# Kernel tuning notes

Hardware: AMD Instinct MI355X
Metric: run time of the kernel (lower is better)

## Reference

```python
import jax, jax.numpy as jnp
import numpy as np

D = 128      # dim_hidden
L = 8        # topological levels (level 0 = primary inputs)
M = 32768    # nodes per level
N = L * M
G = 5        # gate types: maj/not/and/or/xor -> 5 param sets
F = 2        # fan-in per gate node


def setup_inputs() -> dict:
    key = jax.random.key(0)
    ks = jax.random.split(key, 18)
    p = lambda k, sh: jax.random.normal(k, sh, jnp.float32) * 0.05
    return {
        's': jax.random.normal(ks[0], (N, D), jnp.float32),
        't': jax.random.normal(ks[1], (N, D), jnp.float32),
        'gate': jax.random.randint(ks[2], (N,), 0, G, jnp.int32),
        'fanin': jax.random.randint(ks[3], (L - 1, M, F), 0, M, jnp.int32),
        'hs_W': p(ks[4], (2 * D, D)), 'hs_b': p(ks[5], (D,)),
        'aggr_W1': p(ks[6], (G, 2 * D, D)), 'aggr_b1': p(ks[7], (G, D)),
        'aggr_W2': p(ks[8], (G, D, D)), 'aggr_b2': p(ks[9], (G, D)),
        'aggr_W3': p(ks[10], (G, D, D)), 'aggr_b3': p(ks[11], (G, D)),
        'gru_Wi': p(ks[12], (G, D, 3 * D)), 'gru_Wh': p(ks[13], (G, D, 3 * D)),
        'gru_bi': p(ks[14], (G, 3 * D)), 'gru_bh': p(ks[15], (G, 3 * D)),
    }


def _forward(s, t, gate, fanin, hs_W, hs_b, aggr_W1, aggr_b1, aggr_W2, aggr_b2,
             aggr_W3, aggr_b3, gru_Wi, gru_Wh, gru_bi, gru_bh):
    hs = jnp.concatenate([s, t], -1) @ hs_W + hs_b          # [N,D]
    hf = jnp.zeros((N, D), hs.dtype)                        # functional state, zero-init
    for lvl in range(1, L):                                 # level-synchronous sweep
        lo = lvl * M
        g_l = gate[lo:lo + M]                               # [M] gate type of dst nodes
        oh = jax.nn.one_hot(g_l, G, dtype=hs.dtype)         # [M,G] gate selector
        src = (lvl - 1) * M + fanin[lvl - 1]                # [M,F] global fan-in indices
        src_state = jnp.concatenate([hs[src], hf[src]], -1)  # [M,F,2D] node_state gather
        # per-gate-type edge MLP (TFMlpAggr): 3-layer MLP on source states, sum over fan-in
        h1 = jax.nn.relu(jnp.einsum('mfc,gcd->gmfd', src_state, aggr_W1) + aggr_b1[:, None, None, :])
        h2 = jax.nn.relu(jnp.einsum('gmfd,gde->gmfe', h1, aggr_W2) + aggr_b2[:, None, None, :])
        m = jnp.einsum('gmfe,gek->gmfk', h2, aggr_W3) + aggr_b3[:, None, None, :]
        msg = jnp.einsum('gmd,mg->md', m.sum(axis=2), oh)   # [M,D] select own gate's aggr
        # per-gate-type GRU update of hf (torch GRU math, seq_len=1)
        h = hf[lo:lo + M]                                   # [M,D]
        gi = jnp.einsum('md,gdk->gmk', msg, gru_Wi) + gru_bi[:, None, :]  # [G,M,3D]
        gh = jnp.einsum('md,gdk->gmk', h, gru_Wh) + gru_bh[:, None, :]
        r = jax.nn.sigmoid(gi[..., :D] + gh[..., :D])
        z = jax.nn.sigmoid(gi[..., D:2 * D] + gh[..., D:2 * D])
        n = jnp.tanh(gi[..., 2 * D:] + r * gh[..., 2 * D:])
        h_new = jnp.einsum('gmd,mg->md', (1.0 - z) * n + z * h[None], oh)
        hf = hf.at[lo:lo + M].set(h_new)                    # scatter-write back
    return hs, hf


def reference(s, t, gate, fanin, hs_W, hs_b, aggr_W1, aggr_b1, aggr_W2, aggr_b2,
              aggr_W3, aggr_b3, gru_Wi, gru_Wh, gru_bi, gru_bh):
    return _forward(s, t, gate, fanin, hs_W, hs_b, aggr_W1, aggr_b1, aggr_W2,
                    aggr_b2, aggr_W3, aggr_b3, gru_Wi, gru_Wh, gru_bi, gru_bh)
```

## Files before the change

kernel.cpp:

```cpp
#include <hip/hip_runtime.h>
#include <hip/hip_bf16.h>

#define DD 128
#define LL 8
#define MM 32768
#define NN (LL*MM)
#define GG 5
#define FF 2
#define SORT_STRIDE 33408

typedef __attribute__((ext_vector_type(8))) short short8;
typedef __attribute__((ext_vector_type(4))) short short4v;
typedef __attribute__((ext_vector_type(4))) float f32x4;

#define MFMA16(a,b,c) __builtin_amdgcn_mfma_f32_16x16x32_bf16((a),(b),(c),0,0,0)

__device__ __forceinline__ short f2bf(float x){
  __hip_bfloat16 h = __float2bfloat16(x);
  return *reinterpret_cast<short*>(&h);
}

__device__ __forceinline__ short8 pack8(f32x4 a, f32x4 b){
  short8 r;
  r[0]=f2bf(a[0]); r[1]=f2bf(a[1]); r[2]=f2bf(a[2]); r[3]=f2bf(a[3]);
  r[4]=f2bf(b[0]); r[5]=f2bf(b[1]); r[6]=f2bf(b[2]); r[7]=f2bf(b[3]);
  return r;
}

__global__ void prep_kernel(const float* __restrict__ hs_W, const float* __restrict__ W1,
                            const float* __restrict__ W2, const float* __restrict__ W3,
                            const float* __restrict__ Wi,
                            short* __restrict__ hsWt, short* __restrict__ W1t,
                            short* __restrict__ W2t, short* __restrict__ W3t,
                            short* __restrict__ Wit, int* __restrict__ cntcur)
{
  if (blockIdx.x == 0 && threadIdx.x < 70) cntcur[threadIdx.x] = 0;
  int u = blockIdx.x*256 + threadIdx.x;
  const float* src; short* dst; int ldw;
  if (u < 4096){
    int i=u, ct=i>>9, kc=(i>>6)&7, lane=i&63;
    src = hs_W + (size_t)(kc*32 + 8*(lane>>4))*128 + ct*16 + (lane&15);
    dst = hsWt + (size_t)i*8; ldw=128;
  } else if (u < 24576){
    int v=u-4096, g=v>>12, i=v&4095, ct=i>>9, kc=(i>>6)&7, lane=i&63;
    src = W1 + (size_t)g*32768 + (size_t)(kc*32 + 8*(lane>>4))*128 + ct*16 + (lane&15);
    dst = W1t + (size_t)g*32768 + i*8; ldw=128;
  } else if (u < 34816){
    int v=u-24576, g=v>>11, i=v&2047, ct=i>>8, kc=(i>>6)&3, lane=i&63;
    src = W2 + (size_t)g*16384 + (size_t)(kc*32 + 8*(lane>>4))*128 + ct*16 + (lane&15);
    dst = W2t + (size_t)g*16384 + i*8; ldw=128;
  } else if (u < 45056){
    int v=u-34816, g=v>>11, i=v&2047, ct=i>>8, kc=(i>>6)&3, lane=i&63;
    src = W3 + (size_t)g*16384 + (size_t)(kc*32 + 8*(lane>>4))*128 + ct*16 + (lane&15);
    dst = W3t + (size_t)g*16384 + i*8; ldw=128;
  } else {
    int v=u-45056, g=v/6144, i=v%6144, ct=i>>8, kc=(i>>6)&3, lane=i&63;
    src = Wi + (size_t)g*49152 + (size_t)(kc*32 + 8*(lane>>4))*384 + ct*16 + (lane&15);
    dst = Wit + (size_t)g*49152 + i*8; ldw=384;
  }
  short8 o;
#pragma unroll
  for (int j=0;j<8;++j) o[j] = f2bf(src[(size_t)j*ldw]);
  *(short8*)dst = o;
}

__global__ void count_kernel(const int* __restrict__ gate, int* __restrict__ cnt){
  __shared__ int lc[GG];
  const int li = blockIdx.x >> 7;
  const int m  = ((blockIdx.x & 127) << 8) + threadIdx.x;
  if (threadIdx.x < GG) lc[threadIdx.x] = 0;
  __syncthreads();
  int g = gate[(li+1)*MM + m];
  atomicAdd(&lc[g], 1);
  __syncthreads();
  if (threadIdx.x < GG && lc[threadIdx.x] > 0)
    atomicAdd(&cnt[li*GG + threadIdx.x], lc[threadIdx.x]);
}

__global__ void offs_kernel(const int* __restrict__ cnt, int* __restrict__ off,
                            int* __restrict__ pend, int* __restrict__ sorted){
  __shared__ int se[35], sp[35];
  const int tid = threadIdx.x;
  if (tid < LL-1){
    int l = tid, o = 0;
    for (int g = 0; g < GG; ++g){
      off[l*GG+g] = o;
      int c = cnt[l*GG+g];
      pend[l*GG+g] = o + c;
      se[l*GG+g] = o + c;
      o += ((c + 31) >> 5) << 5;
      sp[l*GG+g] = o;
    }
  }
  __syncthreads();
  for (int b = 0; b < 35; ++b){
    int l = b / GG;
    for (int i = se[b] + tid; i < sp[b]; i += 256)
      sorted[l*SORT_STRIDE + i] = -1;
  }
}

__global__ void scatter_kernel(const int* __restrict__ gate, const int* __restrict__ off,
                               int* __restrict__ cur, int* __restrict__ sorted){
  __shared__ int lc[GG];
  __shared__ int base[GG];
  const int li = blockIdx.x >> 7;
  const int m  = ((blockIdx.x & 127) << 8) + threadIdx.x;
  if (threadIdx.x < GG) lc[threadIdx.x] = 0;
  __syncthreads();
  int g = gate[(li+1)*MM + m];
  int p = atomicAdd(&lc[g], 1);
  __syncthreads();
  if (threadIdx.x < GG)
    base[threadIdx.x] = atomicAdd(&cur[li*GG + threadIdx.x], lc[threadIdx.x]);
  __syncthreads();
  sorted[li*SORT_STRIDE + off[li*GG+g] + base[g] + p] = m;
}

__global__ __launch_bounds__(256,4) void hs_kernel(
    const float* __restrict__ s, const float* __restrict__ t,
    const short* __restrict__ Wt, const float* __restrict__ b,
    float* __restrict__ hs, short* __restrict__ hs_sh,
    float* __restrict__ hf, short* __restrict__ hf_sh)
{
  __shared__ __align__(16) short Xs[16384];
  const int tid=threadIdx.x, lane=tid&63, w=tid>>6;
  const int l15=lane&15, lq=lane>>4;
  const int row0 = blockIdx.x*64;

  {
    const int r = tid>>2, p = tid&3;
    const float* srow = s + (size_t)(row0+r)*DD;
    const float* trow = t + (size_t)(row0+r)*DD;
    const int rf = r>>4, rl = r&15;
#pragma unroll
    for (int i=0;i<8;++i){
      int u = p + 4*i;
      const float* pp = (u<16) ? (srow + 8*u) : (trow + 8*(u-16));
      short8 v = pack8(*(const f32x4*)pp, *(const f32x4*)(pp+4));
      *(short8*)(Xs + ((rf*8+(u>>2))*64 + (u&3)*16 + rl)*8) = v;
    }
  }

  if (row0 < MM){
    f32x4 zf4 = {0.f,0.f,0.f,0.f};
    short8 zs8 = {0,0,0,0,0,0,0,0};
    const size_t basei = (size_t)row0*DD;
#pragma unroll
    for (int i=tid; i<2048; i+=256) *(f32x4*)(hf + basei + i*4) = zf4;
#pragma unroll
    for (int i=tid; i<1024; i+=256) *(short8*)(hf_sh + basei + i*8) = zs8;
  }
  __syncthreads();

  f32x4 zf = {0.f,0.f,0.f,0.f};
  f32x4 acc[4][2];
#pragma unroll
  for (int rr=0;rr<4;++rr){ acc[rr][0]=zf; acc[rr][1]=zf; }

  const short* Ab = Wt + lane*8;
#pragma unroll
  for (int kc=0;kc<8;++kc){
    short8 a0 = *(const short8*)(Ab + (16*w + kc)*512);
    short8 a1 = *(const short8*)(Ab + (16*w + 8 + kc)*512);
#pragma unroll
    for (int rr=0;rr<4;++rr){
      short8 bx = *(const short8*)(Xs + ((rr*8 + kc)*64 + lane)*8);
      acc[rr][0] = MFMA16(a0, bx, acc[rr][0]);
      acc[rr][1] = MFMA16(a1, bx, acc[rr][1]);
    }
  }

  f32x4 bv0 = *(const f32x4*)(b + 32*w + 4*lq);
  f32x4 bv1 = *(const f32x4*)(b + 32*w + 16 + 4*lq);
#pragma unroll
  for (int rr=0;rr<4;++rr){
    int row = row0 + rr*16 + l15;
#pragma unroll
    for (int q=0;q<2;++q){
      f32x4 bv = q ? bv1 : bv0;
      int col = 32*w + 16*q + 4*lq;
      f32x4 o; short4v pk;
#pragma unroll
      for (int j=0;j<4;++j){ o[j] = acc[rr][q][j] + bv[j]; pk[j] = f2bf(o[j]); }
      *(f32x4*)(hs + (size_t)row*DD + col) = o;
      *(short4v*)(hs_sh + (size_t)row*DD + col) = pk;
    }
  }
}

__global__ __launch_bounds__(256,4) void level_kernel(
    int lvl, float* __restrict__ hfg,
    const short* __restrict__ hs_sh, short* __restrict__ hf_sh,
    const int* __restrict__ fanin,
    const short* __restrict__ W1t, const short* __restrict__ W2t,
    const short* __restrict__ W3t, const short* __restrict__ Wit,
    const float* __restrict__ b1, const float* __restrict__ b2,
    const float* __restrict__ b3, const float* __restrict__ bi,
    const float* __restrict__ bh,
    const int* __restrict__ off, const int* __restrict__ pend,
    const int* __restrict__ sorted)
{
  __shared__ __align__(16) short Xs[16384];
  __shared__ int nodebuf[32];
  __shared__ int srcbuf[64];
  __shared__ int ginfo;

  const int tid=threadIdx.x, lane=tid&63, w=tid>>6;
  const int l15=lane&15, lq=lane>>4;
  const int li = lvl-1;
  const int pos0 = blockIdx.x*32;

  if (tid==0){
    int g=-1;
    for (int q=0;q<GG;++q)
      if (pos0>=off[li*GG+q] && pos0<pend[li*GG+q]){ g=q; break; }
    ginfo=g;
  }
  if (tid<32) nodebuf[tid] = sorted[li*SORT_STRIDE + pos0 + tid];
  if (tid<64){
    int mg = sorted[li*SORT_STRIDE + pos0 + (tid>>1)];
    srcbuf[tid] = (mg>=0) ? li*MM + fanin[((size_t)li*MM+mg)*FF + (tid&1)] : 0;
  }
  __syncthreads();
  const int g = ginfo;
  if (g<0) return;

  {
    const int r = tid>>2, p = tid&3;
    const int src = srcbuf[r];
    const short* hsrow = hs_sh + (size_t)src*DD;
    const short* hfrow = hf_sh + (size_t)src*DD;
    const int rf = r>>4, rl = r&15;
#pragma unroll
    for (int i=0;i<8;++i){
      int u = p + 4*i;
      short8 v = *(const short8*)((u<16) ? (hsrow + 8*u) : (hfrow + 8*(u-16)));
      *(short8*)(Xs + ((rf*8+(u>>2))*64 + (u&3)*16 + rl)*8) = v;
    }
  }
  __syncthreads();

  f32x4 zf = {0.f,0.f,0.f,0.f};

  f32x4 acc[4][2];
#pragma unroll
  for (int rr=0;rr<4;++rr){ acc[rr][0]=zf; acc[rr][1]=zf; }
  const short* A1 = W1t + (size_t)g*32768 + lane*8;
#pragma unroll
  for (int kc=0;kc<8;++kc){
    short8 a0 = *(const short8*)(A1 + (16*w + kc)*512);
    short8 a1 = *(const short8*)(A1 + (16*w + 8 + kc)*512);
#pragma unroll
    for (int rr=0;rr<4;++rr){
      short8 bx = *(const short8*)(Xs + ((rr*8 + kc)*64 + lane)*8);
      acc[rr][0] = MFMA16(a0, bx, acc[rr][0]);
      acc[rr][1] = MFMA16(a1, bx, acc[rr][1]);
    }
  }
  __syncthreads();
  {
    f32x4 bv0 = *(const f32x4*)(b1 + g*DD + 32*w + 4*lq);
    f32x4 bv1 = *(const f32x4*)(b1 + g*DD + 32*w + 16 + 4*lq);
#pragma unroll
    for (int rr=0;rr<4;++rr){
#pragma unroll
      for (int q=0;q<2;++q){
        f32x4 bv = q ? bv1 : bv0;
        short4v pk;
#pragma unroll
        for (int j=0;j<4;++j) pk[j] = f2bf(fmaxf(acc[rr][q][j] + bv[j], 0.f));
        *(short4v*)(Xs + ((rr*4 + w)*64 + (2*q + (lq>>1))*16 + l15)*8 + 4*(lq&1)) = pk;
      }
    }
  }
  __syncthreads();

  f32x4 acc2[4][2];
#pragma unroll
  for (int rr=0;rr<4;++rr){ acc2[rr][0]=zf; acc2[rr][1]=zf; }
  const short* A2 = W2t + (size_t)g*16384 + lane*8;
#pragma unroll
  for (int kc=0;kc<4;++kc){
    short8 a0 = *(const short8*)(A2 + (8*w + kc)*512);
    short8 a1 = *(const short8*)(A2 + (8*w + 4 + kc)*512);
#pragma unroll
    for (int rr=0;rr<4;++rr){
      short8 bx = *(const short8*)(Xs + ((rr*4 + kc)*64 + lane)*8);
      acc2[rr][0] = MFMA16(a0, bx, acc2[rr][0]);
      acc2[rr][1] = MFMA16(a1, bx, acc2[rr][1]);
    }
  }
  {
    f32x4 bv0 = *(const f32x4*)(b2 + g*DD + 32*w + 4*lq);
    f32x4 bv1 = *(const f32x4*)(b2 + g*DD + 32*w + 16 + 4*lq);
#pragma unroll
    for (int rr=0;rr<4;++rr){
#pragma unroll
      for (int q=0;q<2;++q){
        f32x4 bv = q ? bv1 : bv0;
        short4v pk;
#pragma unroll
        for (int j=0;j<4;++j) pk[j] = f2bf(fmaxf(acc2[rr][q][j] + bv[j], 0.f));
        *(short4v*)(Xs + 8192 + ((rr*4 + w)*64 + (2*q + (lq>>1))*16 + l15)*8 + 4*(lq&1)) = pk;
      }
    }
  }
  __syncthreads();

  f32x4 acc3[4][2];
#pragma unroll
  for (int rr=0;rr<4;++rr){ acc3[rr][0]=zf; acc3[rr][1]=zf; }
  const short* A3 = W3t + (size_t)g*16384 + lane*8;
#pragma unroll
  for (int kc=0;kc<4;++kc){
    short8 a0 = *(const short8*)(A3 + (8*w + kc)*512);
    short8 a1 = *(const short8*)(A3 + (8*w + 4 + kc)*512);
#pragma unroll
    for (int rr=0;rr<4;++rr){
      short8 bx = *(const short8*)(Xs + 8192 + ((rr*4 + kc)*64 + lane)*8);
      acc3[rr][0] = MFMA16(a0, bx, acc3[rr][0]);
      acc3[rr][1] = MFMA16(a1, bx, acc3[rr][1]);
    }
  }
  {
    f32x4 bv0 = *(const f32x4*)(b3 + g*DD + 32*w + 4*lq);
    f32x4 bv1 = *(const f32x4*)(b3 + g*DD + 32*w + 16 + 4*lq);
#pragma unroll
    for (int rr=0;rr<4;++rr){
#pragma unroll
      for (int q=0;q<2;++q){
        f32x4 bv = q ? bv1 : bv0;
        f32x4 mv;
#pragma unroll
        for (int j=0;j<4;++j){
          float v = acc3[rr][q][j];
          mv[j] = v + __shfl_xor(v, 1) + 2.f*bv[j];
        }
        if ((l15 & 1) == 0){
          int n = rr*8 + (l15>>1);
          short4v pk;
#pragma unroll
          for (int j=0;j<4;++j) pk[j] = f2bf(mv[j]);
          *(short4v*)(Xs + (((n>>4)*4 + w)*64 + (2*q + (lq>>1))*16 + (n&15))*8 + 4*(lq&1)) = pk;
        }
      }
    }
  }
  __syncthreads();

  const short* AW = Wit + (size_t)g*49152 + lane*8;
  const int lo = lvl*MM;
#pragma unroll
  for (int q=0;q<2;++q){
    f32x4 gr[2], gz[2], gn[2];
    gr[0]=zf; gr[1]=zf; gz[0]=zf; gz[1]=zf; gn[0]=zf; gn[1]=zf;
#pragma unroll
    for (int kc=0;kc<4;++kc){
      int cti = ((2*w + q)*4 + kc)*512;
      short8 aR = *(const short8*)(AW + cti);
      short8 aZ = *(const short8*)(AW + 16384 + cti);
      short8 aN = *(const short8*)(AW + 32768 + cti);
#pragma unroll
      for (int rfm=0;rfm<2;++rfm){
        short8 bm = *(const short8*)(Xs + ((rfm*4 + kc)*64 + lane)*8);
        gr[rfm] = MFMA16(aR, bm, gr[rfm]);
        gz[rfm] = MFMA16(aZ, bm, gz[rfm]);
        gn[rfm] = MFMA16(aN, bm, gn[rfm]);
      }
    }
    int col = 32*w + 16*q + 4*lq;
    f32x4 biR = *(const f32x4*)(bi + g*384 + col);
    f32x4 biZ = *(const f32x4*)(bi + g*384 + 128 + col);
    f32x4 biN = *(const f32x4*)(bi + g*384 + 256 + col);
    f32x4 bhR = *(const f32x4*)(bh + g*384 + col);
    f32x4 bhZ = *(const f32x4*)(bh + g*384 + 128 + col);
    f32x4 bhN = *(const f32x4*)(bh + g*384 + 256 + col);
#pragma unroll
    for (int rfm=0;rfm<2;++rfm){
      int m = nodebuf[rfm*16 + l15];
      if (m < 0) continue;
      f32x4 o; short4v pk;
#pragma unroll
      for (int j=0;j<4;++j){
        float xr = gr[rfm][j] + biR[j] + bhR[j];
        float xz = gz[rfm][j] + biZ[j] + bhZ[j];
        float r_ = 1.f/(1.f + __expf(-xr));
        float z_ = 1.f/(1.f + __expf(-xz));
        float xn = gn[rfm][j] + biN[j] + r_*bhN[j];
        float n_ = 2.f/(1.f + __expf(-2.f*xn)) - 1.f;
        o[j] = (1.f - z_)*n_;
        pk[j] = f2bf(o[j]);
      }
      *(f32x4*)(hfg + (size_t)(lo + m)*DD + col) = o;
      *(short4v*)(hf_sh + (size_t)(lo + m)*DD + col) = pk;
    }
  }
}

extern "C" void kernel_launch(void* const* d_in, const int* in_sizes, int n_in,
                              void* d_out, int out_size, void* d_ws, size_t ws_size,
                              hipStream_t stream)
{
  const float* s    = (const float*)d_in[0];
  const float* t    = (const float*)d_in[1];
  const int*   gate = (const int*)d_in[2];
  const int*   fanin= (const int*)d_in[3];
  const float* hs_W = (const float*)d_in[4];
  const float* hs_b = (const float*)d_in[5];
  const float* W1   = (const float*)d_in[6];
  const float* b1   = (const float*)d_in[7];
  const float* W2   = (const float*)d_in[8];
  const float* b2   = (const float*)d_in[9];
  const float* W3   = (const float*)d_in[10];
  const float* b3   = (const float*)d_in[11];
  const float* Wi   = (const float*)d_in[12];
  const float* bi   = (const float*)d_in[14];
  const float* bh   = (const float*)d_in[15];

  float* hs = (float*)d_out;
  float* hf = hs + (size_t)NN*DD;

  int* cnt    = (int*)d_ws;
  int* cur    = cnt + 35;
  int* off    = cnt + 70;
  int* pendv  = cnt + 105;
  int* sorted = cnt + 256;

  short* wbase = (short*)((char*)d_ws + (1<<20));
  short* hsWt = wbase;
  short* W1t  = wbase + 32768;
  short* W2t  = wbase + 196608;
  short* W3t  = wbase + 278528;
  short* Wit  = wbase + 360448;

  short* hs_sh = (short*)((char*)d_ws + (size_t)(8<<20));
  short* hf_sh = hs_sh + (size_t)NN*DD;

  prep_kernel<<<296, 256, 0, stream>>>(hs_W, W1, W2, W3, Wi,
                                       hsWt, W1t, W2t, W3t, Wit, cnt);
  count_kernel<<<896, 256, 0, stream>>>(gate, cnt);
  offs_kernel<<<1, 256, 0, stream>>>(cnt, off, pendv, sorted);
  scatter_kernel<<<896, 256, 0, stream>>>(gate, off, cur, sorted);
  hs_kernel<<<NN/64, 256, 0, stream>>>(s, t, hsWt, hs_b, hs, hs_sh, hf, hf_sh);
  for (int lvl = 1; lvl < LL; ++lvl){
    level_kernel<<<SORT_STRIDE/32, 256, 0, stream>>>(lvl, hf,
        hs_sh, hf_sh, fanin, W1t, W2t, W3t, Wit,
        b1, b2, b3, bi, bh, off, pendv, sorted);
  }
}
```

Before: 405.0 us.

## Fuse all stages into one persistent kernel with software grid barriers

Replaces the chain of prep, count, offsets, scatter, hs and seven per-level launches with a single persistent kernel. Blocks loop over work items and synchronise between dependent phases with an atomic-counter grid barrier. The goal is to remove per-launch overhead and inter-kernel gaps. The cost is spin-wait barriers, a fixed grid sized from occupancy, and a risk of deadlock if not all blocks are co-resident.

```diff
diff --git a/kernel.cpp b/kernel.cpp
--- a/kernel.cpp
+++ b/kernel.cpp
@@ -27,374 +27,371 @@
   return r;
 }
 
-__global__ void prep_kernel(const float* __restrict__ hs_W, const float* __restrict__ W1,
-                            const float* __restrict__ W2, const float* __restrict__ W3,
-                            const float* __restrict__ Wi,
-                            short* __restrict__ hsWt, short* __restrict__ W1t,
-                            short* __restrict__ W2t, short* __restrict__ W3t,
-                            short* __restrict__ Wit, int* __restrict__ cntcur)
-{
-  if (blockIdx.x == 0 && threadIdx.x < 70) cntcur[threadIdx.x] = 0;
-  int u = blockIdx.x*256 + threadIdx.x;
-  const float* src; short* dst; int ldw;
-  if (u < 4096){
-    int i=u, ct=i>>9, kc=(i>>6)&7, lane=i&63;
-    src = hs_W + (size_t)(kc*32 + 8*(lane>>4))*128 + ct*16 + (lane&15);
-    dst = hsWt + (size_t)i*8; ldw=128;
-  } else if (u < 24576){
-    int v=u-4096, g=v>>12, i=v&4095, ct=i>>9, kc=(i>>6)&7, lane=i&63;
-    src = W1 + (size_t)g*32768 + (size_t)(kc*32 + 8*(lane>>4))*128 + ct*16 + (lane&15);
-    dst = W1t + (size_t)g*32768 + i*8; ldw=128;
-  } else if (u < 34816){
-    int v=u-24576, g=v>>11, i=v&2047, ct=i>>8, kc=(i>>6)&3, lane=i&63;
-    src = W2 + (size_t)g*16384 + (size_t)(kc*32 + 8*(lane>>4))*128 + ct*16 + (lane&15);
-    dst = W2t + (size_t)g*16384 + i*8; ldw=128;
-  } else if (u < 45056){
-    int v=u-34816, g=v>>11, i=v&2047, ct=i>>8, kc=(i>>6)&3, lane=i&63;
-    src = W3 + (size_t)g*16384 + (size_t)(kc*32 + 8*(lane>>4))*128 + ct*16 + (lane&15);
-    dst = W3t + (size_t)g*16384 + i*8; ldw=128;
-  } else {
-    int v=u-45056, g=v/6144, i=v%6144, ct=i>>8, kc=(i>>6)&3, lane=i&63;
-    src = Wi + (size_t)g*49152 + (size_t)(kc*32 + 8*(lane>>4))*384 + ct*16 + (lane&15);
-    dst = Wit + (size_t)g*49152 + i*8; ldw=384;
-  }
-  short8 o;
-#pragma unroll
-  for (int j=0;j<8;++j) o[j] = f2bf(src[(size_t)j*ldw]);
-  *(short8*)dst = o;
+__device__ __forceinline__ void gbar(int* bar, int target){
+  __syncthreads();
+  if (threadIdx.x == 0){
+    __threadfence();
+    atomicAdd(bar, 1);
+    while (__hip_atomic_load(bar, __ATOMIC_ACQUIRE, __HIP_MEMORY_SCOPE_AGENT) < target)
+      __builtin_amdgcn_s_sleep(8);
+    __threadfence();
+  }
+  __syncthreads();
 }
 
-__global__ void count_kernel(const int* __restrict__ gate, int* __restrict__ cnt){
-  __shared__ int lc[GG];
-  const int li = blockIdx.x >> 7;
-  const int m  = ((blockIdx.x & 127) << 8) + threadIdx.x;
-  if (threadIdx.x < GG) lc[threadIdx.x] = 0;
-  __syncthreads();
-  int g = gate[(li+1)*MM + m];
-  atomicAdd(&lc[g], 1);
-  __syncthreads();
-  if (threadIdx.x < GG && lc[threadIdx.x] > 0)
-    atomicAdd(&cnt[li*GG + threadIdx.x], lc[threadIdx.x]);
-}
-
-__global__ void offs_kernel(const int* __restrict__ cnt, int* __restrict__ off,
-                            int* __restrict__ pend, int* __restrict__ sorted){
-  __shared__ int se[35], sp[35];
-  const int tid = threadIdx.x;
-  if (tid < LL-1){
-    int l = tid, o = 0;
-    for (int g = 0; g < GG; ++g){
-      off[l*GG+g] = o;
-      int c = cnt[l*GG+g];
-      pend[l*GG+g] = o + c;
-      se[l*GG+g] = o + c;
-      o += ((c + 31) >> 5) << 5;
-      sp[l*GG+g] = o;
-    }
-  }
-  __syncthreads();
-  for (int b = 0; b < 35; ++b){
-    int l = b / GG;
-    for (int i = se[b] + tid; i < sp[b]; i += 256)
-      sorted[l*SORT_STRIDE + i] = -1;
-  }
-}
-
-__global__ void scatter_kernel(const int* __restrict__ gate, const int* __restrict__ off,
-                               int* __restrict__ cur, int* __restrict__ sorted){
-  __shared__ int lc[GG];
-  __shared__ int base[GG];
-  const int li = blockIdx.x >> 7;
-  const int m  = ((blockIdx.x & 127) << 8) + threadIdx.x;
-  if (threadIdx.x < GG) lc[threadIdx.x] = 0;
-  __syncthreads();
-  int g = gate[(li+1)*MM + m];
-  int p = atomicAdd(&lc[g], 1);
-  __syncthreads();
-  if (threadIdx.x < GG)
-    base[threadIdx.x] = atomicAdd(&cur[li*GG + threadIdx.x], lc[threadIdx.x]);
-  __syncthreads();
-  sorted[li*SORT_STRIDE + off[li*GG+g] + base[g] + p] = m;
-}
-
-__global__ __launch_bounds__(256,4) void hs_kernel(
+__global__ __launch_bounds__(256,4) void mega_kernel(
     const float* __restrict__ s, const float* __restrict__ t,
-    const short* __restrict__ Wt, const float* __restrict__ b,
-    float* __restrict__ hs, short* __restrict__ hs_sh,
-    float* __restrict__ hf, short* __restrict__ hf_sh)
-{
-  __shared__ __align__(16) short Xs[16384];
-  const int tid=threadIdx.x, lane=tid&63, w=tid>>6;
-  const int l15=lane&15, lq=lane>>4;
-  const int row0 = blockIdx.x*64;
-
-  {
-    const int r = tid>>2, p = tid&3;
-    const float* srow = s + (size_t)(row0+r)*DD;
-    const float* trow = t + (size_t)(row0+r)*DD;
-    const int rf = r>>4, rl = r&15;
-#pragma unroll
-    for (int i=0;i<8;++i){
-      int u = p + 4*i;
-      const float* pp = (u<16) ? (srow + 8*u) : (trow + 8*(u-16));
-      short8 v = pack8(*(const f32x4*)pp, *(const f32x4*)(pp+4));
-      *(short8*)(Xs + ((rf*8+(u>>2))*64 + (u&3)*16 + rl)*8) = v;
-    }
-  }
-
-  if (row0 < MM){
-    f32x4 zf4 = {0.f,0.f,0.f,0.f};
-    short8 zs8 = {0,0,0,0,0,0,0,0};
-    const size_t basei = (size_t)row0*DD;
-#pragma unroll
-    for (int i=tid; i<2048; i+=256) *(f32x4*)(hf + basei + i*4) = zf4;
-#pragma unroll
-    for (int i=tid; i<1024; i+=256) *(short8*)(hf_sh + basei + i*8) = zs8;
-  }
-  __syncthreads();
-
-  f32x4 zf = {0.f,0.f,0.f,0.f};
-  f32x4 acc[4][2];
-#pragma unroll
-  for (int rr=0;rr<4;++rr){ acc[rr][0]=zf; acc[rr][1]=zf; }
-
-  const short* Ab = Wt + lane*8;
-#pragma unroll
-  for (int kc=0;kc<8;++kc){
-    short8 a0 = *(const short8*)(Ab + (16*w + kc)*512);
-    short8 a1 = *(const short8*)(Ab + (16*w + 8 + kc)*512);
-#pragma unroll
-    for (int rr=0;rr<4;++rr){
-      short8 bx = *(const short8*)(Xs + ((rr*8 + kc)*64 + lane)*8);
-      acc[rr][0] = MFMA16(a0, bx, acc[rr][0]);
-      acc[rr][1] = MFMA16(a1, bx, acc[rr][1]);
-    }
-  }
-
-  f32x4 bv0 = *(const f32x4*)(b + 32*w + 4*lq);
-  f32x4 bv1 = *(const f32x4*)(b + 32*w + 16 + 4*lq);
-#pragma unroll
-  for (int rr=0;rr<4;++rr){
-    int row = row0 + rr*16 + l15;
-#pragma unroll
-    for (int q=0;q<2;++q){
-      f32x4 bv = q ? bv1 : bv0;
-      int col = 32*w + 16*q + 4*lq;
-      f32x4 o; short4v pk;
-#pragma unroll
-      for (int j=0;j<4;++j){ o[j] = acc[rr][q][j] + bv[j]; pk[j] = f2bf(o[j]); }
-      *(f32x4*)(hs + (size_t)row*DD + col) = o;
-      *(short4v*)(hs_sh + (size_t)row*DD + col) = pk;
-    }
-  }
-}
-
-__global__ __launch_bounds__(256,4) void level_kernel(
-    int lvl, float* __restrict__ hfg,
-    const short* __restrict__ hs_sh, short* __restrict__ hf_sh,
-    const int* __restrict__ fanin,
-    const short* __restrict__ W1t, const short* __restrict__ W2t,
-    const short* __restrict__ W3t, const short* __restrict__ Wit,
-    const float* __restrict__ b1, const float* __restrict__ b2,
-    const float* __restrict__ b3, const float* __restrict__ bi,
+    const int* __restrict__ gate, const int* __restrict__ fanin,
+    const float* __restrict__ hs_W, const float* __restrict__ hs_b,
+    const float* __restrict__ W1, const float* __restrict__ b1,
+    const float* __restrict__ W2, const float* __restrict__ b2,
+    const float* __restrict__ W3, const float* __restrict__ b3,
+    const float* __restrict__ Wi, const float* __restrict__ bi,
     const float* __restrict__ bh,
-    const int* __restrict__ off, const int* __restrict__ pend,
-    const int* __restrict__ sorted)
+    float* __restrict__ hs, float* __restrict__ hf,
+    short* __restrict__ hsWt, short* __restrict__ W1t, short* __restrict__ W2t,
+    short* __restrict__ W3t, short* __restrict__ Wit,
+    short* __restrict__ hs_sh, short* __restrict__ hf_sh,
+    int* __restrict__ cnt, int* __restrict__ cur, int* __restrict__ off,
+    int* __restrict__ pend, int* __restrict__ pad_end,
+    int* __restrict__ sorted, int* __restrict__ bar)
 {
   __shared__ __align__(16) short Xs[16384];
   __shared__ int nodebuf[32];
   __shared__ int srcbuf[64];
   __shared__ int ginfo;
 
-  const int tid=threadIdx.x, lane=tid&63, w=tid>>6;
-  const int l15=lane&15, lq=lane>>4;
-  const int li = lvl-1;
-  const int pos0 = blockIdx.x*32;
-
-  if (tid==0){
-    int g=-1;
-    for (int q=0;q<GG;++q)
-      if (pos0>=off[li*GG+q] && pos0<pend[li*GG+q]){ g=q; break; }
-    ginfo=g;
-  }
-  if (tid<32) nodebuf[tid] = sorted[li*SORT_STRIDE + pos0 + tid];
-  if (tid<64){
-    int mg = sorted[li*SORT_STRIDE + pos0 + (tid>>1)];
-    srcbuf[tid] = (mg>=0) ? li*MM + fanin[((size_t)li*MM+mg)*FF + (tid&1)] : 0;
-  }
-  __syncthreads();
-  const int g = ginfo;
-  if (g<0) return;
-
-  {
-    const int r = tid>>2, p = tid&3;
-    const int src = srcbuf[r];
-    const short* hsrow = hs_sh + (size_t)src*DD;
-    const short* hfrow = hf_sh + (size_t)src*DD;
-    const int rf = r>>4, rl = r&15;
-#pragma unroll
-    for (int i=0;i<8;++i){
-      int u = p + 4*i;
-      short8 v = *(const short8*)((u<16) ? (hsrow + 8*u) : (hfrow + 8*(u-16)));
-      *(short8*)(Xs + ((rf*8+(u>>2))*64 + (u&3)*16 + rl)*8) = v;
-    }
-  }
-  __syncthreads();
-
+  const int blk = blockIdx.x, NB = gridDim.x;
+  const int tid = threadIdx.x, lane = tid & 63, w = tid >> 6;
+  const int l15 = lane & 15, lq = lane >> 4;
   f32x4 zf = {0.f,0.f,0.f,0.f};
 
-  f32x4 acc[4][2];
-#pragma unroll
-  for (int rr=0;rr<4;++rr){ acc[rr][0]=zf; acc[rr][1]=zf; }
-  const short* A1 = W1t + (size_t)g*32768 + lane*8;
-#pragma unroll
-  for (int kc=0;kc<8;++kc){
-    short8 a0 = *(const short8*)(A1 + (16*w + kc)*512);
-    short8 a1 = *(const short8*)(A1 + (16*w + 8 + kc)*512);
+  for (int u = blk*256 + tid; u < 75776; u += NB*256){
+    const float* src; short* dst; int ldw;
+    if (u < 4096){
+      int i=u, ct=i>>9, kc=(i>>6)&7, ln=i&63;
+      src = hs_W + (size_t)(kc*32 + 8*(ln>>4))*128 + ct*16 + (ln&15);
+      dst = hsWt + (size_t)i*8; ldw=128;
+    } else if (u < 24576){
+      int v=u-4096, g=v>>12, i=v&4095, ct=i>>9, kc=(i>>6)&7, ln=i&63;
+      src = W1 + (size_t)g*32768 + (size_t)(kc*32 + 8*(ln>>4))*128 + ct*16 + (ln&15);
+      dst = W1t + (size_t)g*32768 + i*8; ldw=128;
+    } else if (u < 34816){
+      int v=u-24576, g=v>>11, i=v&2047, ct=i>>8, kc=(i>>6)&3, ln=i&63;
+      src = W2 + (size_t)g*16384 + (size_t)(kc*32 + 8*(ln>>4))*128 + ct*16 + (ln&15);
+      dst = W2t + (size_t)g*16384 + i*8; ldw=128;
+    } else if (u < 45056){
+      int v=u-34816, g=v>>11, i=v&2047, ct=i>>8, kc=(i>>6)&3, ln=i&63;
+      src = W3 + (size_t)g*16384 + (size_t)(kc*32 + 8*(ln>>4))*128 + ct*16 + (ln&15);
+      dst = W3t + (size_t)g*16384 + i*8; ldw=128;
+    } else {
+      int v=u-45056, g=v/6144, i=v%6144, ct=i>>8, kc=(i>>6)&3, ln=i&63;
+      src = Wi + (size_t)g*49152 + (size_t)(kc*32 + 8*(ln>>4))*384 + ct*16 + (ln&15);
+      dst = Wit + (size_t)g*49152 + i*8; ldw=384;
+    }
+    short8 o;
+#pragma unroll
+    for (int j=0;j<8;++j) o[j] = f2bf(src[(size_t)j*ldw]);
+    *(short8*)dst = o;
+  }
+  for (int c0 = blk; c0 < 896; c0 += NB){
+    int* lc = (int*)Xs;
+    __syncthreads();
+    if (tid < GG) lc[tid] = 0;
+    __syncthreads();
+    int idx = c0*256 + tid;
+    int li = idx >> 15, m = idx & 32767;
+    int g = gate[(li+1)*MM + m];
+    atomicAdd(&lc[g], 1);
+    __syncthreads();
+    if (tid < GG && lc[tid] > 0) atomicAdd(&cnt[li*GG + tid], lc[tid]);
+  }
+  gbar(bar, NB*1);
+
+  if (blk < LL-1){
+    int* lds_i = (int*)Xs;
+    if (tid == 0){
+      int l = blk, o = 0;
+      for (int g2 = 0; g2 < GG; ++g2){
+        off[l*GG+g2] = o;
+        int c = cnt[l*GG+g2];
+        pend[l*GG+g2] = o + c;
+        lds_i[g2] = o + c;
+        o += ((c + 31) >> 5) << 5;
+        lds_i[8+g2] = o;
+      }
+      pad_end[l] = o;
+    }
+    __syncthreads();
+    for (int b2 = 0; b2 < GG; ++b2)
+      for (int i = lds_i[b2] + tid; i < lds_i[8+b2]; i += 256)
+        sorted[blk*SORT_STRIDE + i] = -1;
+  }
+  gbar(bar, NB*2);
+
+  for (int c0 = blk; c0 < 896; c0 += NB){
+    int* lc = (int*)Xs; int* base = lc + 8;
+    __syncthreads();
+    if (tid < GG) lc[tid] = 0;
+    __syncthreads();
+    int idx = c0*256 + tid;
+    int li = idx >> 15, m = idx & 32767;
+    int g = gate[(li+1)*MM + m];
+    int p = atomicAdd(&lc[g], 1);
+    __syncthreads();
+    if (tid < GG) base[tid] = atomicAdd(&cur[li*GG + tid], lc[tid]);
+    __syncthreads();
+    sorted[li*SORT_STRIDE + off[li*GG+g] + base[g] + p] = m;
+  }
+  for (int it = blk; it < 4096; it += NB){
+    const int row0 = it*64;
+    __syncthreads();
+    {
+      const int r = tid>>2, p = tid&3;
+      const float* srow = s + (size_t)(row0+r)*DD;
+      const float* trow = t + (size_t)(row0+r)*DD;
+      const int rf = r>>4, rl = r&15;
+#pragma unroll
+      for (int i=0;i<8;++i){
+        int u = p + 4*i;
+        const float* pp = (u<16) ? (srow + 8*u) : (trow + 8*(u-16));
+        short8 v = pack8(*(const f32x4*)pp, *(const f32x4*)(pp+4));
+        *(short8*)(Xs + ((rf*8+(u>>2))*64 + (u&3)*16 + rl)*8) = v;
+      }
+    }
+    if (row0 < MM){
+      short8 zs8 = {0,0,0,0,0,0,0,0};
+      const size_t basei = (size_t)row0*DD;
+      for (int i=tid; i<2048; i+=256) *(f32x4*)(hf + basei + i*4) = zf;
+      for (int i=tid; i<1024; i+=256) *(short8*)(hf_sh + basei + i*8) = zs8;
+    }
+    __syncthreads();
+
+    f32x4 acc[4][2];
+#pragma unroll
+    for (int rr=0;rr<4;++rr){ acc[rr][0]=zf; acc[rr][1]=zf; }
+    const short* Ab = hsWt + lane*8;
+#pragma unroll
+    for (int kc=0;kc<8;++kc){
+      short8 a0 = *(const short8*)(Ab + (16*w + kc)*512);
+      short8 a1 = *(const short8*)(Ab + (16*w + 8 + kc)*512);
+#pragma unroll
+      for (int rr=0;rr<4;++rr){
+        short8 bx = *(const short8*)(Xs + ((rr*8 + kc)*64 + lane)*8);
+        acc[rr][0] = MFMA16(a0, bx, acc[rr][0]);
+        acc[rr][1] = MFMA16(a1, bx, acc[rr][1]);
+      }
+    }
+    f32x4 bv0 = *(const f32x4*)(hs_b + 32*w + 4*lq);
+    f32x4 bv1 = *(const f32x4*)(hs_b + 32*w + 16 + 4*lq);
 #pragma unroll
     for (int rr=0;rr<4;++rr){
-      short8 bx = *(const short8*)(Xs + ((rr*8 + kc)*64 + lane)*8);
-      acc[rr][0] = MFMA16(a0, bx, acc[rr][0]);
-      acc[rr][1] = MFMA16(a1, bx, acc[rr][1]);
-    }
-  }
-  __syncthreads();
-  {
-    f32x4 bv0 = *(const f32x4*)(b1 + g*DD + 32*w + 4*lq);
-    f32x4 bv1 = *(const f32x4*)(b1 + g*DD + 32*w + 16 + 4*lq);
-#pragma unroll
-    for (int rr=0;rr<4;++rr){
+      int row = row0 + rr*16 + l15;
 #pragma unroll
       for (int q=0;q<2;++q){
         f32x4 bv = q ? bv1 : bv0;
-        short4v pk;
-#pragma unroll
-        for (int j=0;j<4;++j) pk[j] = f2bf(fmaxf(acc[rr][q][j] + bv[j], 0.f));
-        *(short4v*)(Xs + ((rr*4 + w)*64 + (2*q + (lq>>1))*16 + l15)*8 + 4*(lq&1)) = pk;
-      }
-    }
-  }
-  __syncthreads();
-
-  f32x4 acc2[4][2];
-#pragma unroll
-  for (int rr=0;rr<4;++rr){ acc2[rr][0]=zf; acc2[rr][1]=zf; }
-  const short* A2 = W2t + (size_t)g*16384 + lane*8;
-#pragma unroll
-  for (int kc=0;kc<4;++kc){
-    short8 a0 = *(const short8*)(A2 + (8*w + kc)*512);
-    short8 a1 = *(const short8*)(A2 + (8*w + 4 + kc)*512);
-#pragma unroll
-    for (int rr=0;rr<4;++rr){
-      short8 bx = *(const short8*)(Xs + ((rr*4 + kc)*64 + lane)*8);
-      acc2[rr][0] = MFMA16(a0, bx, acc2[rr][0]);
-      acc2[rr][1] = MFMA16(a1, bx, acc2[rr][1]);
-    }
-  }
-  {
-    f32x4 bv0 = *(const f32x4*)(b2 + g*DD + 32*w + 4*lq);
-    f32x4 bv1 = *(const f32x4*)(b2 + g*DD + 32*w + 16 + 4*lq);
-#pragma unroll
-    for (int rr=0;rr<4;++rr){
-#pragma unroll
-      for (int q=0;q<2;++q){
-        f32x4 bv = q ? bv1 : bv0;
-        short4v pk;
-#pragma unroll
-        for (int j=0;j<4;++j) pk[j] = f2bf(fmaxf(acc2[rr][q][j] + bv[j], 0.f));
-        *(short4v*)(Xs + 8192 + ((rr*4 + w)*64 + (2*q + (lq>>1))*16 + l15)*8 + 4*(lq&1)) = pk;
-      }
-    }
-  }
-  __syncthreads();
-
-  f32x4 acc3[4][2];
-#pragma unroll
-  for (int rr=0;rr<4;++rr){ acc3[rr][0]=zf; acc3[rr][1]=zf; }
-  const short* A3 = W3t + (size_t)g*16384 + lane*8;
-#pragma unroll
-  for (int kc=0;kc<4;++kc){
-    short8 a0 = *(const short8*)(A3 + (8*w + kc)*512);
-    short8 a1 = *(const short8*)(A3 + (8*w + 4 + kc)*512);
-#pragma unroll
-    for (int rr=0;rr<4;++rr){
-      short8 bx = *(const short8*)(Xs + 8192 + ((rr*4 + kc)*64 + lane)*8);
-      acc3[rr][0] = MFMA16(a0, bx, acc3[rr][0]);
-      acc3[rr][1] = MFMA16(a1, bx, acc3[rr][1]);
-    }
-  }
-  {
-    f32x4 bv0 = *(const f32x4*)(b3 + g*DD + 32*w + 4*lq);
-    f32x4 bv1 = *(const f32x4*)(b3 + g*DD + 32*w + 16 + 4*lq);
-#pragma unroll
-    for (int rr=0;rr<4;++rr){
-#pragma unroll
-      for (int q=0;q<2;++q){
-        f32x4 bv = q ? bv1 : bv0;
-        f32x4 mv;
-#pragma unroll
-        for (int j=0;j<4;++j){
-          float v = acc3[rr][q][j];
-          mv[j] = v + __shfl_xor(v, 1) + 2.f*bv[j];
-        }
-        if ((l15 & 1) == 0){
-          int n = rr*8 + (l15>>1);
-          short4v pk;
-#pragma unroll
-          for (int j=0;j<4;++j) pk[j] = f2bf(mv[j]);
-          *(short4v*)(Xs + (((n>>4)*4 + w)*64 + (2*q + (lq>>1))*16 + (n&15))*8 + 4*(lq&1)) = pk;
-        }
-      }
-    }
-  }
-  __syncthreads();
-
-  const short* AW = Wit + (size_t)g*49152 + lane*8;
-  const int lo = lvl*MM;
-#pragma unroll
-  for (int q=0;q<2;++q){
-    f32x4 gr[2], gz[2], gn[2];
-    gr[0]=zf; gr[1]=zf; gz[0]=zf; gz[1]=zf; gn[0]=zf; gn[1]=zf;
-#pragma unroll
-    for (int kc=0;kc<4;++kc){
-      int cti = ((2*w + q)*4 + kc)*512;
-      short8 aR = *(const short8*)(AW + cti);
-      short8 aZ = *(const short8*)(AW + 16384 + cti);
-      short8 aN = *(const short8*)(AW + 32768 + cti);
-#pragma unroll
-      for (int rfm=0;rfm<2;++rfm){
-        short8 bm = *(const short8*)(Xs + ((rfm*4 + kc)*64 + lane)*8);
-        gr[rfm] = MFMA16(aR, bm, gr[rfm]);
-        gz[rfm] = MFMA16(aZ, bm, gz[rfm]);
-        gn[rfm] = MFMA16(aN, bm, gn[rfm]);
-      }
-    }
-    int col = 32*w + 16*q + 4*lq;
-    f32x4 biR = *(const f32x4*)(bi + g*384 + col);
-    f32x4 biZ = *(const f32x4*)(bi + g*384 + 128 + col);
-    f32x4 biN = *(const f32x4*)(bi + g*384 + 256 + col);
-    f32x4 bhR = *(const f32x4*)(bh + g*384 + col);
-    f32x4 bhZ = *(const f32x4*)(bh + g*384 + 128 + col);
-    f32x4 bhN = *(const f32x4*)(bh + g*384 + 256 + col);
-#pragma unroll
-    for (int rfm=0;rfm<2;++rfm){
-      int m = nodebuf[rfm*16 + l15];
-      if (m < 0) continue;
-      f32x4 o; short4v pk;
-#pragma unroll
-      for (int j=0;j<4;++j){
-        float xr = gr[rfm][j] + biR[j] + bhR[j];
-        float xz = gz[rfm][j] + biZ[j] + bhZ[j];
-        float r_ = 1.f/(1.f + __expf(-xr));
-        float z_ = 1.f/(1.f + __expf(-xz));
-        float xn = gn[rfm][j] + biN[j] + r_*bhN[j];
-        float n_ = 2.f/(1.f + __expf(-2.f*xn)) - 1.f;
-        o[j] = (1.f - z_)*n_;
-        pk[j] = f2bf(o[j]);
-      }
-      *(f32x4*)(hfg + (size_t)(lo + m)*DD + col) = o;
-      *(short4v*)(hf_sh + (size_t)(lo + m)*DD + col) = pk;
-    }
+        int col = 32*w + 16*q + 4*lq;
+        f32x4 o; short4v pk;
+#pragma unroll
+        for (int j=0;j<4;++j){ o[j] = acc[rr][q][j] + bv[j]; pk[j] = f2bf(o[j]); }
+        *(f32x4*)(hs + (size_t)row*DD + col) = o;
+        *(short4v*)(hs_sh + (size_t)row*DD + col) = pk;
+      }
+    }
+  }
+  gbar(bar, NB*3);
+
+  for (int lvl = 1; lvl < LL; ++lvl){
+    const int li = lvl-1;
+    const int pe = pad_end[li];
+    for (int it = blk; it*32 < pe; it += NB){
+      const int pos0 = it*32;
+      __syncthreads();
+      if (tid==0){
+        int g=-1;
+        for (int q=0;q<GG;++q)
+          if (pos0>=off[li*GG+q] && pos0<pend[li*GG+q]){ g=q; break; }
+        ginfo=g;
+      }
+      if (tid<32) nodebuf[tid] = sorted[li*SORT_STRIDE + pos0 + tid];
+      if (tid<64){
+        int mg = sorted[li*SORT_STRIDE + pos0 + (tid>>1)];
+        srcbuf[tid] = (mg>=0) ? li*MM + fanin[((size_t)li*MM+mg)*FF + (tid&1)] : 0;
+      }
+      __syncthreads();
+      const int g = ginfo;
+      if (g >= 0){
+        {
+          const int r = tid>>2, p = tid&3;
+          const int src = srcbuf[r];
+          const short* hsrow = hs_sh + (size_t)src*DD;
+          const short* hfrow = hf_sh + (size_t)src*DD;
+          const int rf = r>>4, rl = r&15;
+#pragma unroll
+          for (int i=0;i<8;++i){
+            int u = p + 4*i;
+            short8 v = *(const short8*)((u<16) ? (hsrow + 8*u) : (hfrow + 8*(u-16)));
+            *(short8*)(Xs + ((rf*8+(u>>2))*64 + (u&3)*16 + rl)*8) = v;
+          }
+        }
+        __syncthreads();
+
+        f32x4 acc[4][2];
+#pragma unroll
+        for (int rr=0;rr<4;++rr){ acc[rr][0]=zf; acc[rr][1]=zf; }
+        const short* A1 = W1t + (size_t)g*32768 + lane*8;
+#pragma unroll
+        for (int kc=0;kc<8;++kc){
+          short8 a0 = *(const short8*)(A1 + (16*w + kc)*512);
+          short8 a1 = *(const short8*)(A1 + (16*w + 8 + kc)*512);
+#pragma unroll
+          for (int rr=0;rr<4;++rr){
+            short8 bx = *(const short8*)(Xs + ((rr*8 + kc)*64 + lane)*8);
+            acc[rr][0] = MFMA16(a0, bx, acc[rr][0]);
+            acc[rr][1] = MFMA16(a1, bx, acc[rr][1]);
+          }
+        }
+        __syncthreads();
+        {
+          f32x4 bv0 = *(const f32x4*)(b1 + g*DD + 32*w + 4*lq);
+          f32x4 bv1 = *(const f32x4*)(b1 + g*DD + 32*w + 16 + 4*lq);
+#pragma unroll
+          for (int rr=0;rr<4;++rr){
+#pragma unroll
+            for (int q=0;q<2;++q){
+              f32x4 bv = q ? bv1 : bv0;
+              short4v pk;
+#pragma unroll
+              for (int j=0;j<4;++j) pk[j] = f2bf(fmaxf(acc[rr][q][j] + bv[j], 0.f));
+              *(short4v*)(Xs + ((rr*4 + w)*64 + (2*q + (lq>>1))*16 + l15)*8 + 4*(lq&1)) = pk;
+            }
+          }
+        }
+        __syncthreads();
+
+        f32x4 acc2[4][2];
+#pragma unroll
+        for (int rr=0;rr<4;++rr){ acc2[rr][0]=zf; acc2[rr][1]=zf; }
+        const short* A2 = W2t + (size_t)g*16384 + lane*8;
+#pragma unroll
+        for (int kc=0;kc<4;++kc){
+          short8 a0 = *(const short8*)(A2 + (8*w + kc)*512);
+          short8 a1 = *(const short8*)(A2 + (8*w + 4 + kc)*512);
+#pragma unroll
+          for (int rr=0;rr<4;++rr){
+            short8 bx = *(const short8*)(Xs + ((rr*4 + kc)*64 + lane)*8);
+            acc2[rr][0] = MFMA16(a0, bx, acc2[rr][0]);
+            acc2[rr][1] = MFMA16(a1, bx, acc2[rr][1]);
+          }
+        }
+        {
+          f32x4 bv0 = *(const f32x4*)(b2 + g*DD + 32*w + 4*lq);
+          f32x4 bv1 = *(const f32x4*)(b2 + g*DD + 32*w + 16 + 4*lq);
+#pragma unroll
+          for (int rr=0;rr<4;++rr){
+#pragma unroll
+            for (int q=0;q<2;++q){
+              f32x4 bv = q ? bv1 : bv0;
+              short4v pk;
+#pragma unroll
+              for (int j=0;j<4;++j) pk[j] = f2bf(fmaxf(acc2[rr][q][j] + bv[j], 0.f));
+              *(short4v*)(Xs + 8192 + ((rr*4 + w)*64 + (2*q + (lq>>1))*16 + l15)*8 + 4*(lq&1)) = pk;
+            }
+          }
+        }
+        __syncthreads();
+
+        f32x4 acc3[4][2];
+#pragma unroll
+        for (int rr=0;rr<4;++rr){ acc3[rr][0]=zf; acc3[rr][1]=zf; }
+        const short* A3 = W3t + (size_t)g*16384 + lane*8;
+#pragma unroll
+        for (int kc=0;kc<4;++kc){
+          short8 a0 = *(const short8*)(A3 + (8*w + kc)*512);
+          short8 a1 = *(const short8*)(A3 + (8*w + 4 + kc)*512);
+#pragma unroll
+          for (int rr=0;rr<4;++rr){
+            short8 bx = *(const short8*)(Xs + 8192 + ((rr*4 + kc)*64 + lane)*8);
+            acc3[rr][0] = MFMA16(a0, bx, acc3[rr][0]);
+            acc3[rr][1] = MFMA16(a1, bx, acc3[rr][1]);
+          }
+        }
+        {
+          f32x4 bv0 = *(const f32x4*)(b3 + g*DD + 32*w + 4*lq);
+          f32x4 bv1 = *(const f32x4*)(b3 + g*DD + 32*w + 16 + 4*lq);
+#pragma unroll
+          for (int rr=0;rr<4;++rr){
+#pragma unroll
+            for (int q=0;q<2;++q){
+              f32x4 bv = q ? bv1 : bv0;
+              f32x4 mv;
+#pragma unroll
+              for (int j=0;j<4;++j){
+                float v = acc3[rr][q][j];
+                mv[j] = v + __shfl_xor(v, 1) + 2.f*bv[j];
+              }
+              if ((l15 & 1) == 0){
+                int n = rr*8 + (l15>>1);
+                short4v pk;
+#pragma unroll
+                for (int j=0;j<4;++j) pk[j] = f2bf(mv[j]);
+                *(short4v*)(Xs + (((n>>4)*4 + w)*64 + (2*q + (lq>>1))*16 + (n&15))*8 + 4*(lq&1)) = pk;
+              }
+            }
+          }
+        }
+        __syncthreads();
+
+        const short* AW = Wit + (size_t)g*49152 + lane*8;
+        const int lo = lvl*MM;
+#pragma unroll
+        for (int q=0;q<2;++q){
+          f32x4 gr[2], gz[2], gn[2];
+          gr[0]=zf; gr[1]=zf; gz[0]=zf; gz[1]=zf; gn[0]=zf; gn[1]=zf;
+#pragma unroll
+          for (int kc=0;kc<4;++kc){
+            int cti = ((2*w + q)*4 + kc)*512;
+            short8 aR = *(const short8*)(AW + cti);
+            short8 aZ = *(const short8*)(AW + 16384 + cti);
+            short8 aN = *(const short8*)(AW + 32768 + cti);
+#pragma unroll
+            for (int rfm=0;rfm<2;++rfm){
+              short8 bm = *(const short8*)(Xs + ((rfm*4 + kc)*64 + lane)*8);
+              gr[rfm] = MFMA16(aR, bm, gr[rfm]);
+              gz[rfm] = MFMA16(aZ, bm, gz[rfm]);
+              gn[rfm] = MFMA16(aN, bm, gn[rfm]);
+            }
+          }
+          int col = 32*w + 16*q + 4*lq;
+          f32x4 biR = *(const f32x4*)(bi + g*384 + col);
+          f32x4 biZ = *(const f32x4*)(bi + g*384 + 128 + col);
+          f32x4 biN = *(const f32x4*)(bi + g*384 + 256 + col);
+          f32x4 bhR = *(const f32x4*)(bh + g*384 + col);
+          f32x4 bhZ = *(const f32x4*)(bh + g*384 + 128 + col);
+          f32x4 bhN = *(const f32x4*)(bh + g*384 + 256 + col);
+#pragma unroll
+          for (int rfm=0;rfm<2;++rfm){
+            int m = nodebuf[rfm*16 + l15];
+            if (m < 0) continue;
+            f32x4 o; short4v pk;
+#pragma unroll
+            for (int j=0;j<4;++j){
+              float xr = gr[rfm][j] + biR[j] + bhR[j];
+              float xz = gz[rfm][j] + biZ[j] + bhZ[j];
+              float r_ = 1.f/(1.f + __expf(-xr));
+              float z_ = 1.f/(1.f + __expf(-xz));
+              float xn = gn[rfm][j] + biN[j] + r_*bhN[j];
+              float n_ = 2.f/(1.f + __expf(-2.f*xn)) - 1.f;
+              o[j] = (1.f - z_)*n_;
+              pk[j] = f2bf(o[j]);
+            }
+            *(f32x4*)(hf + (size_t)(lo + m)*DD + col) = o;
+            *(short4v*)(hf_sh + (size_t)(lo + m)*DD + col) = pk;
+          }
+        }
+      }
+    }
+    if (lvl < LL-1) gbar(bar, NB*(3+lvl));
   }
 }
 
@@ -421,11 +418,13 @@
   float* hs = (float*)d_out;
   float* hf = hs + (size_t)NN*DD;
 
-  int* cnt    = (int*)d_ws;
-  int* cur    = cnt + 35;
-  int* off    = cnt + 70;
-  int* pendv  = cnt + 105;
-  int* sorted = cnt + 256;
+  int* cnt     = (int*)d_ws;
+  int* cur     = cnt + 35;
+  int* off     = cnt + 70;
+  int* pendv   = cnt + 105;
+  int* pad_end = cnt + 140;
+  int* bar     = cnt + 160;
+  int* sorted  = cnt + 256;
 
   short* wbase = (short*)((char*)d_ws + (1<<20));
   short* hsWt = wbase;
@@ -437,15 +436,15 @@
   short* hs_sh = (short*)((char*)d_ws + (size_t)(8<<20));
   short* hf_sh = hs_sh + (size_t)NN*DD;
 
-  prep_kernel<<<296, 256, 0, stream>>>(hs_W, W1, W2, W3, Wi,
-                                       hsWt, W1t, W2t, W3t, Wit, cnt);
-  count_kernel<<<896, 256, 0, stream>>>(gate, cnt);
-  offs_kernel<<<1, 256, 0, stream>>>(cnt, off, pendv, sorted);
-  scatter_kernel<<<896, 256, 0, stream>>>(gate, off, cur, sorted);
-  hs_kernel<<<NN/64, 256, 0, stream>>>(s, t, hsWt, hs_b, hs, hs_sh, hf, hf_sh);
-  for (int lvl = 1; lvl < LL; ++lvl){
-    level_kernel<<<SORT_STRIDE/32, 256, 0, stream>>>(lvl, hf,
-        hs_sh, hf_sh, fanin, W1t, W2t, W3t, Wit,
-        b1, b2, b3, bi, bh, off, pendv, sorted);
-  }
+  int nper = 0;
+  hipOccupancyMaxActiveBlocksPerMultiprocessor(&nper, mega_kernel, 256, 0);
+  if (nper < 1) nper = 1;
+  int NBLK = nper * 256;
+  if (NBLK > 1024) NBLK = 1024;
+
+  hipMemsetAsync(d_ws, 0, 1024, stream);
+  mega_kernel<<<NBLK, 256, 0, stream>>>(
+      s, t, gate, fanin, hs_W, hs_b, W1, b1, W2, b2, W3, b3, Wi, bi, bh,
+      hs, hf, hsWt, W1t, W2t, W3t, Wit, hs_sh, hf_sh,
+      cnt, cur, off, pendv, pad_end, sorted, bar);
 }
```

Measured after the change: 1.502 ms. 3.71x slower.
